# Optimization experiments

Measured on AMD Instinct MI355X. Metric: run time of the kernel, lower is better.

## Reference

```python
import jax, jax.numpy as jnp
import numpy as np
import math

B, T, EMB, HD = 4, 2048, 2048, 128
HALF = HD // 2


def setup_inputs() -> dict:
    key = jax.random.key(0)
    ks = jax.random.split(key, 4)
    x = jax.random.normal(ks[0], (B, T, EMB), dtype=jnp.float32)
    s = 1.0 / math.sqrt(EMB)
    Wq = jax.random.normal(ks[1], (EMB, HD), dtype=jnp.float32) * s
    Wk = jax.random.normal(ks[2], (EMB, HD), dtype=jnp.float32) * s
    Wv = jax.random.normal(ks[3], (EMB, HD), dtype=jnp.float32) * s
    # Standard RoPE rotation table: theta_i = 10000^(-2i/HD), angle = pos * theta
    inv_freq = 1.0 / (10000.0 ** (np.arange(0, HALF, dtype=np.float32) / HALF))
    angles = np.arange(T, dtype=np.float32)[:, None] * inv_freq[None, :]  # [T, HALF]
    rot_cos = jnp.asarray(np.cos(angles), dtype=jnp.float32)
    rot_sin = jnp.asarray(np.sin(angles), dtype=jnp.float32)
    # Additive causal mask: 0 on/below diagonal, -1e9 above
    NEG = -1e9
    mask = jnp.where(jnp.tril(jnp.ones((T, T), dtype=bool)), 0.0, NEG).astype(jnp.float32)
    return {"x": x, "Wq": Wq, "Wk": Wk, "Wv": Wv,
            "rot_cos": rot_cos, "rot_sin": rot_sin, "mask": mask}


def _apply_rope(q, rot_cos, rot_sin):
    # q: [B, T, HD]; view last dim as HALF complex pairs and rotate
    qp = q.reshape(q.shape[0], q.shape[1], HALF, 2)
    re, im = qp[..., 0], qp[..., 1]
    out_re = re * rot_cos - im * rot_sin  # broadcast [T,HALF] over batch
    out_im = re * rot_sin + im * rot_cos
    return jnp.stack([out_re, out_im], axis=-1).reshape(q.shape)


def reference(x, Wq, Wk, Wv, rot_cos, rot_sin, mask):
    Q = x @ Wq  # [B, T, HD]
    K = x @ Wk
    V = x @ Wv
    Q = _apply_rope(Q, rot_cos, rot_sin)
    K = _apply_rope(K, rot_cos, rot_sin)
    scores = jnp.einsum('bqd,bkd->bqk', Q, K) / math.sqrt(HD)
    probs = jax.nn.softmax(scores + mask, axis=-1)  # dropout is identity in eval
    return jnp.einsum('bqk,bkd->bqd', probs, V)
```

## Files before the change

kernel.cpp:

```cpp
#include <hip/hip_runtime.h>
#include <cstddef>
#include <cstdint>

#define T_SEQ 2048
#define EMB_D 2048
#define HD_D  128

typedef __attribute__((ext_vector_type(8))) short short8;
typedef __attribute__((ext_vector_type(4))) float f32x4;
typedef __attribute__((ext_vector_type(4))) unsigned short ushort4v;
typedef __attribute__((ext_vector_type(8))) unsigned short ushort8v;
typedef __attribute__((ext_vector_type(2))) unsigned int uint2v;

static __device__ __forceinline__ unsigned short f2bf_rne(float f) {
    union { float f; unsigned u; } v; v.f = f;
    unsigned r = v.u + 0x7fffu + ((v.u >> 16) & 1u);
    return (unsigned short)(r >> 16);
}
static __device__ __forceinline__ unsigned short f2bf_fast(float f) {
    union { float f; unsigned u; } v; v.f = f;
    return (unsigned short)((v.u + 0x8000u) >> 16);
}
static __device__ __forceinline__ float bf2f(unsigned short h) {
    union { unsigned u; float f; } v; v.u = ((unsigned)h) << 16;
    return v.f;
}
static __device__ __forceinline__ unsigned pk2(float a, float b) {
    union { float f; unsigned u; } x, y; x.f = a; y.f = b;
    return __builtin_amdgcn_perm(y.u + 0x8000u, x.u + 0x8000u, 0x07060302);
}
#define EXP2F(x) __builtin_amdgcn_exp2f(x)

__global__ __launch_bounds__(256) void prep_weights(
    const float* __restrict__ Wq, const float* __restrict__ Wk,
    const float* __restrict__ Wv, unsigned short* __restrict__ Wt)
{
    __shared__ __attribute__((aligned(16))) unsigned short tw[64 * 132];
    const int w = blockIdx.y;
    const int k0 = blockIdx.x * 64;
    const float* W = (w == 0) ? Wq : (w == 1) ? Wk : Wv;
    const int tid = threadIdx.x;
#pragma unroll
    for (int p = 0; p < 8; p++) {
        const int f = p * 256 + tid;
        const int row = f >> 5, c4 = f & 31;
        const float4 v = *(const float4*)&W[(size_t)(k0 + row) * HD_D + c4 * 4];
        ushort4v h = { f2bf_rne(v.x), f2bf_rne(v.y), f2bf_rne(v.z), f2bf_rne(v.w) };
        *(ushort4v*)&tw[row * 132 + c4 * 4] = h;
    }
    __syncthreads();
    const int kk = (tid & 7) * 8;
#pragma unroll
    for (int p = 0; p < 4; p++) {
        const int n = p * 32 + (tid >> 3);
        ushort8v o;
#pragma unroll
        for (int jj = 0; jj < 8; jj++) o[jj] = tw[(kk + jj) * 132 + n];
        *(ushort8v*)&Wt[(size_t)w * (HD_D * EMB_D) + (size_t)n * EMB_D + k0 + kk] = o;
    }
}

__global__ __launch_bounds__(256, 2) void qkv_fused(
    const float* __restrict__ x, const unsigned short* __restrict__ Wt,
    const float* __restrict__ rcos, const float* __restrict__ rsin,
    unsigned short* __restrict__ Qb, unsigned short* __restrict__ Kb,
    unsigned short* __restrict__ Vt)
{
    __shared__ __attribute__((aligned(16))) unsigned short xsm[2][64 * 64];
    __shared__ __attribute__((aligned(16))) unsigned short wsm[2][96 * 64];
    const int L = blockIdx.x;
    const int xcd = L & 7, s = L >> 3;
    const int ng = s & 3;
    const int m0 = (xcd * 16 + (s >> 2)) * 64;
    const int tid = threadIdx.x;
    const int lane = tid & 63, wave = tid >> 6;
    const int wm = wave >> 1, wn = wave & 1;
    const int l15 = lane & 15, lq = lane >> 4;

    const int xrow = tid >> 4, xc = tid & 15;
    const float* xsrc = x + (size_t)(m0 + xrow) * EMB_D + xc * 4;
    const int wrow = tid >> 3, wc = tid & 7;
    const unsigned short* wsrc = Wt + (size_t)(ng * 96 + wrow) * EMB_D + wc * 8;

    const int xw  = xrow * 128 + (((xc >> 1) ^ (xrow & 7)) << 4) + (xc & 1) * 8;
    const int wwo = wrow * 128 + ((wc ^ (wrow & 7)) << 4);

    int ra[2][2], rb[3][2];
#pragma unroll
    for (int i = 0; i < 2; i++)
#pragma unroll
        for (int ks = 0; ks < 2; ks++) {
            const int row = wm * 32 + i * 16 + l15;
            ra[i][ks] = row * 128 + (((ks * 4 + lq) ^ (row & 7)) << 4);
        }
#pragma unroll
    for (int jj = 0; jj < 3; jj++)
#pragma unroll
        for (int ks = 0; ks < 2; ks++) {
            const int row = wn * 48 + jj * 16 + l15;
            rb[jj][ks] = row * 128 + (((ks * 4 + lq) ^ (row & 7)) << 4);
        }

    f32x4 acc[2][3];
#pragma unroll
    for (int i = 0; i < 2; i++)
#pragma unroll
        for (int j = 0; j < 3; j++) acc[i][j] = (f32x4){0.f, 0.f, 0.f, 0.f};

    float4 xr[2][4];
    short8 wr[2][3];

#define LOADN(SET, K)                                                             \
    do {                                                                          \
        _Pragma("unroll")                                                         \
        for (int p = 0; p < 4; p++)                                               \
            xr[SET][p] = *(const float4*)(xsrc + (size_t)p * (16 * EMB_D) + (K)); \
        _Pragma("unroll")                                                         \
        for (int p = 0; p < 3; p++)                                               \
            wr[SET][p] = *(const short8*)(wsrc + (size_t)p * (32 * EMB_D) + (K)); \
    } while (0)

#define STAGE(SET, BUF)                                                           \
    do {                                                                          \
        char* xb = (char*)&xsm[BUF][0];                                           \
        char* wb = (char*)&wsm[BUF][0];                                           \
        _Pragma("unroll")                                                         \
        for (int p = 0; p < 4; p++) {                                             \
            uint2v u;                                                             \
            u.x = pk2(xr[SET][p].x, xr[SET][p].y);                                \
            u.y = pk2(xr[SET][p].z, xr[SET][p].w);                                \
            *(uint2v*)(xb + xw + p * 2048) = u;                                   \
        }                                                                         \
        _Pragma("unroll")                                                         \
        for (int p = 0; p < 3; p++)                                               \
            *(short8*)(wb + wwo + p * 4096) = wr[SET][p];                         \
    } while (0)

#define COMPUTE(BUF)                                                              \
    do {                                                                          \
        const char* xb = (const char*)&xsm[BUF][0];                               \
        const char* wb = (const char*)&wsm[BUF][0];                               \
        short8 Af[2][2];                                                          \
        _Pragma("unroll")                                                         \
        for (int i = 0; i < 2; i++)                                               \
            _Pragma("unroll")                                                     \
            for (int ks = 0; ks < 2; ks++)                                        \
                Af[i][ks] = *(const short8*)(xb + ra[i][ks]);                     \
        __builtin_amdgcn_s_setprio(1);                                            \
        _Pragma("unroll")                                                         \
        for (int ks = 0; ks < 2; ks++)                                            \
            _Pragma("unroll")                                                     \
            for (int jj = 0; jj < 3; jj++) {                                      \
                const short8 Bf = *(const short8*)(wb + rb[jj][ks]);              \
                _Pragma("unroll")                                                 \
                for (int i = 0; i < 2; i++)                                       \
                    acc[i][jj] = __builtin_amdgcn_mfma_f32_16x16x32_bf16(         \
                        Af[i][ks], Bf, acc[i][jj], 0, 0, 0);                      \
            }                                                                     \
        __builtin_amdgcn_s_setprio(0);                                            \
    } while (0)

#define BARX() asm volatile("s_waitcnt lgkmcnt(0)\n\ts_barrier" ::: "memory")

    LOADN(0, 0);
    LOADN(1, 64);
    STAGE(0, 0);
    LOADN(0, 128);

#pragma clang loop unroll(disable)
    for (int j = 0; j < 28; j += 2) {
        BARX(); STAGE(1, 1); LOADN(1, (j + 3) * 64); COMPUTE(0);
        BARX(); STAGE(0, 0); LOADN(0, (j + 4) * 64); COMPUTE(1);
    }
    BARX(); STAGE(1, 1); LOADN(1, 31 * 64); COMPUTE(0);
    BARX(); STAGE(0, 0);                    COMPUTE(1);
    BARX(); STAGE(1, 1);                    COMPUTE(0);
    BARX();                                 COMPUTE(1);

#undef LOADN
#undef STAGE
#undef COMPUTE
#undef BARX

    const float qscale = 0.08838834764831845f * 1.4426950408889634f;
#pragma unroll
    for (int i = 0; i < 2; i++) {
#pragma unroll
        for (int r = 0; r < 4; r++) {
            const int row = m0 + wm * 32 + i * 16 + lq * 4 + r;
            const int t = row & (T_SEQ - 1);
            const int bb = row >> 11;
#pragma unroll
            for (int j = 0; j < 3; j++) {
                const int col = ng * 96 + wn * 48 + j * 16 + l15;
                const int mat = col >> 7, mcol = col & 127;
                const float v = acc[i][j][r];
                if (mat == 2) {
                    Vt[((size_t)bb * HD_D + mcol) * T_SEQ + t] = f2bf_rne(v);
                } else {
                    const int ip = mcol >> 1;
                    const float c = rcos[t * 64 + ip];
                    const float s2 = rsin[t * 64 + ip];
                    const float pv = __shfl_xor(v, 1);
                    float rv = (mcol & 1) ? (pv * s2 + v * c) : (v * c - pv * s2);
                    if (mat == 0) {
                        rv *= qscale;
                        Qb[(size_t)row * HD_D + mcol] = f2bf_rne(rv);
                    } else {
                        Kb[(size_t)row * HD_D + mcol] = f2bf_rne(rv);
                    }
                }
            }
        }
    }
}

__global__ __launch_bounds__(256, 2) void attn(
    const unsigned short* __restrict__ Qb, const unsigned short* __restrict__ Kb,
    const unsigned short* __restrict__ Vt, float* __restrict__ O0,
    unsigned short* __restrict__ O1, float* __restrict__ Lp)
{
    __shared__ __attribute__((aligned(16))) unsigned short O_s[4][32 * 128];
    __shared__ __attribute__((aligned(16))) unsigned short P_s[4][32 * 40];
    __shared__ float l_s[4][32];

    const int tid = threadIdx.x;
    const int lane = tid & 63, wave = tid >> 6;
    const int l15 = lane & 15, lq = lane >> 4;
    const int kf = lq * 8;

    const int L = blockIdx.x;
    const int g = L & 1;
    const int b = (L >> 1) & 3;
    const int q0 = (63 - (L >> 3)) * 32;
    const int kend = q0 + 32;
    const float M2 = 16.0f;

    const unsigned short* Qp = Qb + (size_t)(b * T_SEQ + q0) * HD_D;
    short8 aQ[2][4];
#pragma unroll
    for (int i = 0; i < 2; i++)
#pragma unroll
        for (int d = 0; d < 4; d++)
            aQ[i][d] = *(const short8*)&Qp[(size_t)(i * 16 + l15) * HD_D + d * 32 + kf];

    f32x4 acc[2][8];
#pragma unroll
    for (int i = 0; i < 2; i++)
#pragma unroll
        for (int d = 0; d < 8; d++) acc[i][d] = (f32x4){0.f, 0.f, 0.f, 0.f};
    float l_r[2][4] = {{0.f, 0.f, 0.f, 0.f}, {0.f, 0.f, 0.f, 0.f}};

    const unsigned short* Kbase = Kb + (size_t)b * T_SEQ * HD_D;
    const unsigned short* Vbase = Vt + (size_t)b * HD_D * T_SEQ;
    unsigned short* Pw = &P_s[wave][0];

    short8 KA_A[8], KA_B[8], VA[8];
    f32x4 sc[2][2];

#define LOADK(DST, C0)                                                         \
    do {                                                                       \
        const unsigned short* Kp = Kbase + (size_t)((C0) * 32) * HD_D;         \
        _Pragma("unroll")                                                      \
        for (int d = 0; d < 4; d++)                                            \
            _Pragma("unroll")                                                  \
            for (int n = 0; n < 2; n++)                                        \
                DST[d * 2 + n] =                                               \
                    *(const short8*)&Kp[(size_t)(n * 16 + l15) * HD_D + d * 32 + kf]; \
    } while (0)

#define QKSEG(KREG)                                                            \
    do {                                                                       \
        _Pragma("unroll")                                                      \
        for (int i = 0; i < 2; i++)                                            \
            _Pragma("unroll")                                                  \
            for (int n = 0; n < 2; n++) sc[i][n] = (f32x4){0.f, 0.f, 0.f, 0.f};\
        _Pragma("unroll")                                                      \
        for (int d = 0; d < 4; d++)                                            \
            _Pragma("unroll")                                                  \
            for (int i = 0; i < 2; i++)                                        \
                _Pragma("unroll")                                              \
                for (int n = 0; n < 2; n++)                                    \
                    sc[i][n] = __builtin_amdgcn_mfma_f32_16x16x32_bf16(        \
                        aQ[i][d], KREG[d * 2 + n], sc[i][n], 0, 0, 0);         \
    } while (0)

#define LOADV(C0)                                                              \
    do {                                                                       \
        _Pragma("unroll")                                                      \
        for (int d = 0; d < 8; d++)                                            \
            VA[d] = *(const short8*)                                           \
                &Vbase[(size_t)(d * 16 + l15) * T_SEQ + (C0) * 32 + kf];       \
    } while (0)

#define SMPV(C0)                                                               \
    do {                                                                       \
        const int kA = (C0) * 32;                                              \
        _Pragma("unroll")                                                      \
        for (int i = 0; i < 2; i++)                                            \
            _Pragma("unroll")                                                  \
            for (int r = 0; r < 4; r++) {                                      \
                const int q = q0 + i * 16 + lq * 4 + r;                        \
                const float p0 = ((kA + l15)      <= q) ? EXP2F(sc[i][0][r] - M2) : 0.f; \
                const float p1 = ((kA + 16 + l15) <= q) ? EXP2F(sc[i][1][r] - M2) : 0.f; \
                l_r[i][r] += p0 + p1;                                          \
                const int prow = (i * 16 + lq * 4 + r) * 40;                   \
                Pw[prow + l15]      = f2bf_fast(p0);                           \
                Pw[prow + 16 + l15] = f2bf_fast(p1);                           \
            }                                                                  \
        short8 pA[2];                                                          \
        _Pragma("unroll")                                                      \
        for (int i = 0; i < 2; i++)                                            \
            pA[i] = *(const short8*)&Pw[(i * 16 + l15) * 40 + kf];             \
        _Pragma("unroll")                                                      \
        for (int i = 0; i < 2; i++)                                            \
            _Pragma("unroll")                                                  \
            for (int d = 0; d < 8; d++)                                        \
                acc[i][d] = __builtin_amdgcn_mfma_f32_16x16x32_bf16(           \
                    pA[i], VA[d], acc[i][d], 0, 0, 0);                         \
    } while (0)

    int cc = 2 * wave + g;
    if (cc * 32 < kend) {
        LOADK(KA_A, cc);
#pragma clang loop unroll(disable)
        for (;;) {
            QKSEG(KA_A);
            LOADV(cc);
            {
                const int cB = cc + 8;
                const bool hB = (cB * 32 < kend);
                if (hB) LOADK(KA_B, cB);
                SMPV(cc);
                if (!hB) break;
            }
            QKSEG(KA_B);
            LOADV(cc + 8);
            {
                const int cC = cc + 16;
                const bool hC = (cC * 32 < kend);
                if (hC) LOADK(KA_A, cC);
                SMPV(cc + 8);
                if (!hC) break;
            }
            cc += 16;
        }
    }

#undef LOADK
#undef QKSEG
#undef LOADV
#undef SMPV

#pragma unroll
    for (int i = 0; i < 2; i++)
#pragma unroll
        for (int r = 0; r < 4; r++) {
            float lr = l_r[i][r];
            lr += __shfl_xor(lr, 1);
            lr += __shfl_xor(lr, 2);
            lr += __shfl_xor(lr, 4);
            lr += __shfl_xor(lr, 8);
            if (l15 == 0) l_s[wave][i * 16 + lq * 4 + r] = lr;
#pragma unroll
            for (int d = 0; d < 8; d++)
                O_s[wave][(i * 16 + lq * 4 + r) * 128 + d * 16 + l15] = f2bf_fast(acc[i][d][r]);
        }
    __syncthreads();

#pragma unroll
    for (int pass = 0; pass < 2; pass++) {
        const int row = pass * 16 + (tid >> 4);
        const int dc = (tid & 15) * 8;
        const float lt = l_s[0][row] + l_s[1][row] + l_s[2][row] + l_s[3][row];
        float o[8];
#pragma unroll
        for (int k = 0; k < 8; k++) o[k] = 0.f;
#pragma unroll
        for (int w2 = 0; w2 < 4; w2++) {
            const ushort8v pv = *(const ushort8v*)&O_s[w2][row * 128 + dc];
#pragma unroll
            for (int k = 0; k < 8; k++) o[k] += bf2f(pv[k]);
        }
        const size_t grow = (size_t)(b * T_SEQ + q0 + row);
        if (g == 0) {
            float* op = O0 + grow * HD_D + dc;
#pragma unroll
            for (int k = 0; k < 8; k++) op[k] = o[k];
        } else {
            ushort8v h;
#pragma unroll
            for (int k = 0; k < 8; k++) h[k] = f2bf_fast(o[k]);
            *(ushort8v*)&O1[grow * HD_D + dc] = h;
        }
        if ((tid & 15) == 0) Lp[g * 8192 + grow] = lt;
    }
}

__global__ __launch_bounds__(256) void attn_merge(
    float* __restrict__ out, const unsigned short* __restrict__ O1,
    const float* __restrict__ Lp)
{
    const int idx = blockIdx.x * 256 + threadIdx.x;
    const int row = idx >> 5;
    f32x4 a = ((f32x4*)out)[idx];
    const ushort4v h = ((const ushort4v*)O1)[idx];
    f32x4 bv = { bf2f(h.x), bf2f(h.y), bf2f(h.z), bf2f(h.w) };
    const float inv = 1.0f / (Lp[row] + Lp[8192 + row]);
    ((f32x4*)out)[idx] = (a + bv) * inv;
}

extern "C" void kernel_launch(void* const* d_in, const int* in_sizes, int n_in,
                              void* d_out, int out_size, void* d_ws, size_t ws_size,
                              hipStream_t stream)
{
    (void)in_sizes; (void)n_in; (void)out_size; (void)ws_size;
    const float* x  = (const float*)d_in[0];
    const float* Wq = (const float*)d_in[1];
    const float* Wk = (const float*)d_in[2];
    const float* Wv = (const float*)d_in[3];
    const float* rc = (const float*)d_in[4];
    const float* rs = (const float*)d_in[5];
    float* out = (float*)d_out;

    char* ws = (char*)d_ws;
    unsigned short* Wt = (unsigned short*)(ws);
    unsigned short* Qb = (unsigned short*)(ws + 1572864);
    unsigned short* Kb = (unsigned short*)(ws + 3670016);
    unsigned short* Vt = (unsigned short*)(ws + 5767168);
    unsigned short* O1 = (unsigned short*)(ws + 7864320);
    float*          Lp = (float*)(ws + 9961472);

    prep_weights<<<dim3(32, 3), 256, 0, stream>>>(Wq, Wk, Wv, Wt);
    qkv_fused   <<<dim3(512),   256, 0, stream>>>(x, Wt, rc, rs, Qb, Kb, Vt);
    attn        <<<dim3(512),   256, 0, stream>>>(Qb, Kb, Vt, out, O1, Lp);
    attn_merge  <<<dim3(1024),  256, 0, stream>>>(out, O1, Lp);
}
```

Measured before the change: 172.4 us.

## Fuse split-K merge into attention kernel via last-arriver atomic counter

Removes the separate attn_merge launch. Each attention block now bumps a per-(batch, query-tile) atomic counter, and the second of the two split blocks to finish reads both partial outputs and the row sums and writes the normalized result. The counter array is zeroed in prep_weights and reset after each merge. This saves a kernel launch and a full pass over the output, at the cost of thread fences, an atomic, and tail work inside the attention kernel.

```diff
diff --git a/kernel.cpp b/kernel.cpp
--- a/kernel.cpp
+++ b/kernel.cpp
@@ -33,13 +33,15 @@
 
 __global__ __launch_bounds__(256) void prep_weights(
     const float* __restrict__ Wq, const float* __restrict__ Wk,
-    const float* __restrict__ Wv, unsigned short* __restrict__ Wt)
+    const float* __restrict__ Wv, unsigned short* __restrict__ Wt,
+    int* __restrict__ Cnt)
 {
     __shared__ __attribute__((aligned(16))) unsigned short tw[64 * 132];
     const int w = blockIdx.y;
     const int k0 = blockIdx.x * 64;
     const float* W = (w == 0) ? Wq : (w == 1) ? Wk : Wv;
     const int tid = threadIdx.x;
+    if (blockIdx.x == 0 && blockIdx.y == 0) Cnt[tid] = 0;
 #pragma unroll
     for (int p = 0; p < 8; p++) {
         const int f = p * 256 + tid;
@@ -218,11 +220,13 @@
 __global__ __launch_bounds__(256, 2) void attn(
     const unsigned short* __restrict__ Qb, const unsigned short* __restrict__ Kb,
     const unsigned short* __restrict__ Vt, float* __restrict__ O0,
-    unsigned short* __restrict__ O1, float* __restrict__ Lp)
+    unsigned short* __restrict__ O1, float* __restrict__ Lp,
+    int* __restrict__ Cnt)
 {
     __shared__ __attribute__((aligned(16))) unsigned short O_s[4][32 * 128];
     __shared__ __attribute__((aligned(16))) unsigned short P_s[4][32 * 40];
     __shared__ float l_s[4][32];
+    __shared__ int do_merge;
 
     const int tid = threadIdx.x;
     const int lane = tid & 63, wave = tid >> 6;
@@ -232,7 +236,8 @@
     const int L = blockIdx.x;
     const int g = L & 1;
     const int b = (L >> 1) & 3;
-    const int q0 = (63 - (L >> 3)) * 32;
+    const int qb = L >> 3;
+    const int q0 = (63 - qb) * 32;
     const int kend = q0 + 32;
     const float M2 = 16.0f;
 
@@ -395,19 +400,30 @@
         }
         if ((tid & 15) == 0) Lp[g * 8192 + grow] = lt;
     }
-}
-
-__global__ __launch_bounds__(256) void attn_merge(
-    float* __restrict__ out, const unsigned short* __restrict__ O1,
-    const float* __restrict__ Lp)
-{
-    const int idx = blockIdx.x * 256 + threadIdx.x;
-    const int row = idx >> 5;
-    f32x4 a = ((f32x4*)out)[idx];
-    const ushort4v h = ((const ushort4v*)O1)[idx];
-    f32x4 bv = { bf2f(h.x), bf2f(h.y), bf2f(h.z), bf2f(h.w) };
-    const float inv = 1.0f / (Lp[row] + Lp[8192 + row]);
-    ((f32x4*)out)[idx] = (a + bv) * inv;
+
+    __threadfence();
+    __syncthreads();
+    if (tid == 0) {
+        const int old = atomicAdd(&Cnt[(b << 6) + qb], 1);
+        do_merge = (old == 1);
+    }
+    __syncthreads();
+    if (do_merge) {
+        __threadfence();
+        const size_t rbase = (size_t)(b * T_SEQ + q0);
+#pragma unroll
+        for (int p = 0; p < 4; p++) {
+            const int e = p * 256 + tid;
+            const int row = e >> 5, c4 = e & 31;
+            const size_t grow = rbase + row;
+            f32x4 a = *(const f32x4*)&O0[grow * HD_D + c4 * 4];
+            const ushort4v h = *(const ushort4v*)&O1[grow * HD_D + c4 * 4];
+            f32x4 bv = { bf2f(h.x), bf2f(h.y), bf2f(h.z), bf2f(h.w) };
+            const float inv = 1.0f / (Lp[grow] + Lp[8192 + grow]);
+            *(f32x4*)&O0[grow * HD_D + c4 * 4] = (a + bv) * inv;
+        }
+        if (tid == 0) Cnt[(b << 6) + qb] = 0;
+    }
 }
 
 extern "C" void kernel_launch(void* const* d_in, const int* in_sizes, int n_in,
@@ -430,9 +446,9 @@
     unsigned short* Vt = (unsigned short*)(ws + 5767168);
     unsigned short* O1 = (unsigned short*)(ws + 7864320);
     float*          Lp = (float*)(ws + 9961472);
-
-    prep_weights<<<dim3(32, 3), 256, 0, stream>>>(Wq, Wk, Wv, Wt);
+    int*            Ct = (int*)(ws + 10027008);
+
+    prep_weights<<<dim3(32, 3), 256, 0, stream>>>(Wq, Wk, Wv, Wt, Ct);
     qkv_fused   <<<dim3(512),   256, 0, stream>>>(x, Wt, rc, rs, Qb, Kb, Vt);
-    attn        <<<dim3(512),   256, 0, stream>>>(Qb, Kb, Vt, out, O1, Lp);
-    attn_merge  <<<dim3(1024),  256, 0, stream>>>(out, O1, Lp);
-}
+    attn        <<<dim3(512),   256, 0, stream>>>(Qb, Kb, Vt, out, O1, Lp, Ct);
+}
```

After: 310.2 us. +79.9%, slower.
